# Kernel tuning notes

Hardware: AMD Instinct MI355X
Metric: run time of the kernel (lower is better)

The kernel has to match this reference:

```python
import jax, jax.numpy as jnp
import numpy as np

B, T, C = 8, 1024, 1024   # batch, seq (== block_size), n_embed
H, D = 16, 64             # num_heads, head_size


def setup_inputs() -> dict:
    key = jax.random.key(0)
    kx, kq, kk, kv = jax.random.split(key, 4)
    scale = C ** -0.5  # mimic nn.Linear init scale roughly
    return {
        "x": jax.random.normal(kx, (B, T, C), dtype=jnp.float32),
        "Wq": jax.random.normal(kq, (H, C, D), dtype=jnp.float32) * scale,
        "Wk": jax.random.normal(kk, (H, C, D), dtype=jnp.float32) * scale,
        "Wv": jax.random.normal(kv, (H, C, D), dtype=jnp.float32) * scale,
    }


def reference(x, Wq, Wk, Wv):
    # Per-head Q/K/V projections (batched over heads instead of a Python loop)
    q = jnp.einsum("btc,hcd->bhtd", x, Wq)
    k = jnp.einsum("btc,hcd->bhtd", x, Wk)
    v = jnp.einsum("btc,hcd->bhtd", x, Wv)

    # scaled causal attention scores: [B, H, T, T]
    scores = jnp.einsum("bhtd,bhsd->bhts", q, k) * (D ** -0.5)
    causal = jnp.tril(jnp.ones((T, T), dtype=bool))
    scores = jnp.where(causal, scores, jnp.finfo(scores.dtype).min)
    attn = jax.nn.softmax(scores, axis=-1)

    out = jnp.einsum("bhts,bhsd->bhtd", attn, v)  # [B, H, T, D]
    # concat heads along last dim -> [B, T, H*D]
    return out.transpose(0, 2, 1, 3).reshape(B, T, H * D)
```

## Files before the change

kernel.cpp:

```cpp
#include <hip/hip_runtime.h>
#include <hip/hip_bf16.h>
#include <cstdint>


typedef __attribute__((ext_vector_type(8))) short short8;
typedef __attribute__((ext_vector_type(4))) short bfs4;
typedef __attribute__((ext_vector_type(4))) float f32x4;

typedef const __attribute__((address_space(1))) void* gas1_t;
typedef __attribute__((address_space(3))) void* las3_t;

__device__ __forceinline__ void gl_lds16(const void* g, void* l) {
  __builtin_amdgcn_global_load_lds((gas1_t)g, (las3_t)l, 16, 0, 0);
}

__device__ __forceinline__ unsigned short f2bf(float f) {
  union { float f; unsigned int u; } v; v.f = f;
  unsigned int u = v.u;
  return (unsigned short)((u + 0x7fffu + ((u >> 16) & 1u)) >> 16);
}

__device__ __forceinline__ unsigned int pk_bf16(float a, float b) {
  union { __hip_bfloat162 h; unsigned int u; } cv;
  cv.h = __float22bfloat162_rn(make_float2(a, b));
  return cv.u;
}

__global__ __launch_bounds__(256) void k_convert_x(const float* __restrict__ x,
                                                   unsigned short* __restrict__ xb) {
  int g = blockIdx.x * 256 + threadIdx.x;
  const float4* xp = (const float4*)x + (size_t)g * 2;
  float4 a = xp[0], b = xp[1];
  short8 o;
  o[0] = (short)f2bf(a.x); o[1] = (short)f2bf(a.y);
  o[2] = (short)f2bf(a.z); o[3] = (short)f2bf(a.w);
  o[4] = (short)f2bf(b.x); o[5] = (short)f2bf(b.y);
  o[6] = (short)f2bf(b.z); o[7] = (short)f2bf(b.w);
  *(short8*)(xb + (size_t)g * 8) = o;
}

__global__ __launch_bounds__(256) void k_convert_w(const float* __restrict__ Wq,
                                                   const float* __restrict__ Wk,
                                                   const float* __restrict__ Wv,
                                                   unsigned short* __restrict__ Wt) {
  int g = blockIdx.x * 256 + threadIdx.x;
  int d  = g & 63;
  int cb = (g >> 6) & 127;
  int h  = (g >> 13) & 15;
  int p  = g >> 17;
  const float* W = (p == 0) ? Wq : (p == 1) ? Wk : Wv;
  const float* src = W + ((size_t)h * 1024 + cb * 8) * 64 + d;
  short8 o;
#pragma unroll
  for (int j = 0; j < 8; ++j) o[j] = (short)f2bf(src[(size_t)j * 64]);
  *(short8*)(Wt + (((size_t)p * 16 + h) * 64 + d) * 1024 + cb * 8) = o;
}

__global__ __launch_bounds__(256) void k_proj(const unsigned short* __restrict__ xb,
                                              const unsigned short* __restrict__ Wt,
                                              unsigned short* __restrict__ Qb,
                                              unsigned short* __restrict__ Kb,
                                              unsigned short* __restrict__ Vt) {
  __shared__ alignas(16) unsigned short As[8192];
  __shared__ alignas(16) unsigned short Bs[8192];
  const int p   = blockIdx.y;
  const int bx  = blockIdx.x;
  const int tid = threadIdx.x;
  const int lane = tid & 63, w = tid >> 6;
  const int ln = lane & 15, quad = lane >> 4;
  const int wm = w >> 1, wn = w & 1;

  const unsigned short* Abase;
  const unsigned short* Bbase;
  int m0, n0;
  const int c = bx & 7, j = bx >> 3;
  if (p < 2) {
    Abase = xb; Bbase = Wt + (size_t)p * 1048576;
    m0 = ((j >> 3) * 8 + c) * 128;
    n0 = (j & 7) * 128;
  } else {
    Abase = Wt + (size_t)2 * 1048576; Bbase = xb;
    n0 = ((j >> 3) * 8 + c) * 128;
    m0 = (j & 7) * 128;
  }

  f32x4 acc[4][4];
#pragma unroll
  for (int i = 0; i < 4; ++i)
#pragma unroll
    for (int jj = 0; jj < 4; ++jj) acc[i][jj] = (f32x4){0.f, 0.f, 0.f, 0.f};

  for (int kt = 0; kt < 16; ++kt) {
    const int c0 = kt * 64;
    __syncthreads();
#pragma unroll
    for (int i = 0; i < 4; ++i) {
      int idx = i * 256 + tid;
      int iln = idx & 15, iq = (idx >> 4) & 3, imt = (idx >> 6) & 7, ikk = (idx >> 9) & 1;
      int row = imt * 16 + iln;
      int col = c0 + ikk * 32 + iq * 8;
      char* la = (char*)As + (size_t)(i * 256 + (tid & ~63)) * 16;
      char* lb = (char*)Bs + (size_t)(i * 256 + (tid & ~63)) * 16;
      gl_lds16(Abase + (size_t)(m0 + row) * 1024 + col, la);
      gl_lds16(Bbase + (size_t)(n0 + row) * 1024 + col, lb);
    }
    __builtin_amdgcn_s_waitcnt(0);
    __syncthreads();

    short8 af[2][4], bfr[2][4];
#pragma unroll
    for (int kk = 0; kk < 2; ++kk)
#pragma unroll
      for (int t4 = 0; t4 < 4; ++t4) {
        af[kk][t4]  = *(const short8*)&As[(size_t)((((kk * 8 + wm * 4 + t4) * 4 + quad) * 16 + ln)) * 8];
        bfr[kk][t4] = *(const short8*)&Bs[(size_t)((((kk * 8 + wn * 4 + t4) * 4 + quad) * 16 + ln)) * 8];
      }
#pragma unroll
    for (int kk = 0; kk < 2; ++kk)
#pragma unroll
      for (int mt = 0; mt < 4; ++mt)
#pragma unroll
        for (int nt = 0; nt < 4; ++nt)
          acc[mt][nt] = __builtin_amdgcn_mfma_f32_16x16x32_bf16(
              af[kk][mt], bfr[kk][nt], acc[mt][nt], 0, 0, 0);
  }

  unsigned short* outp = (p == 0) ? Qb : (p == 1) ? Kb : Vt;
#pragma unroll
  for (int mt = 0; mt < 4; ++mt)
#pragma unroll
    for (int nt = 0; nt < 4; ++nt)
#pragma unroll
      for (int r = 0; r < 4; ++r) {
        int m = m0 + (wm * 4 + mt) * 16 + quad * 4 + r;
        int n = n0 + (wn * 4 + nt) * 16 + ln;
        size_t addr;
        if (p < 2) {
          addr = ((size_t)(m >> 10) * 16 + (n >> 6)) * 65536 + (size_t)(m & 1023) * 64 + (n & 63);
        } else {
          addr = ((size_t)(n >> 10) * 1024 + m) * 1024 + (n & 1023);
        }
        outp[addr] = f2bf(acc[mt][nt][r]);
      }
}

__global__ __launch_bounds__(256) void k_attn(const unsigned short* __restrict__ Qb,
                                              const unsigned short* __restrict__ Kb,
                                              const unsigned short* __restrict__ Vt,
                                              float* __restrict__ out) {
  __shared__ alignas(16) unsigned short Ks[4096];
  __shared__ alignas(16) unsigned short Vs[4096];
  __shared__ alignas(16) unsigned short Ps[8192];
  const int bid = blockIdx.x;
  const int qb = 7 - (bid >> 7);
  const int bh = bid & 127;
  const int b = bh >> 4, h = bh & 15;
  const int tid = threadIdx.x, lane = tid & 63, w = tid >> 6;
  const int ln = lane & 15, quad = lane >> 4;

  short8 qf[2][2];
#pragma unroll
  for (int qt = 0; qt < 2; ++qt) {
    const int q = qb * 128 + qt * 64 + w * 16 + ln;
#pragma unroll
    for (int kk = 0; kk < 2; ++kk)
      qf[qt][kk] = *(const short8*)(Qb + ((size_t)bh * 1024 + q) * 64 + kk * 32 + quad * 8);
  }

  f32x4 o[2][4];
#pragma unroll
  for (int qt = 0; qt < 2; ++qt)
#pragma unroll
    for (int dt = 0; dt < 4; ++dt) o[qt][dt] = (f32x4){0.f, 0.f, 0.f, 0.f};
  float l_i[2] = {0.f, 0.f};
  const float sc = 0.18033688011112042f;
  const float FM = 16.0f;

  const int ktmax = 2 * qb + 1;
  for (int kt = 0; kt <= ktmax; ++kt) {
    const int s0 = kt * 64;
    __syncthreads();
#pragma unroll
    for (int i = 0; i < 2; ++i) {
      int idx = i * 256 + tid;
      int iln = idx & 15, iq = (idx >> 4) & 3, ikk = (idx >> 6) & 1, it = (idx >> 7) & 3;
      char* lk = (char*)Ks + (size_t)(i * 256 + (tid & ~63)) * 16;
      char* lv = (char*)Vs + (size_t)(i * 256 + (tid & ~63)) * 16;
      gl_lds16(Kb + ((size_t)bh * 1024 + s0 + it * 16 + iln) * 64 + ikk * 32 + iq * 8, lk);
      gl_lds16(Vt + ((size_t)bh * 64 + it * 16 + iln) * 1024 + s0 + ikk * 32 + iq * 8, lv);
    }
    __builtin_amdgcn_s_waitcnt(0);
    __syncthreads();

    f32x4 st[2][4];
#pragma unroll
    for (int s = 0; s < 4; ++s) {
      st[0][s] = (f32x4){0.f, 0.f, 0.f, 0.f};
      st[1][s] = (f32x4){0.f, 0.f, 0.f, 0.f};
#pragma unroll
      for (int kk = 0; kk < 2; ++kk) {
        short8 kf = *(const short8*)&Ks[(size_t)(((s * 2 + kk) * 4 + quad) * 16 + ln) * 8];
        st[0][s] = __builtin_amdgcn_mfma_f32_16x16x32_bf16(kf, qf[0][kk], st[0][s], 0, 0, 0);
        st[1][s] = __builtin_amdgcn_mfma_f32_16x16x32_bf16(kf, qf[1][kk], st[1][s], 0, 0, 0);
      }
    }

#pragma unroll
    for (int qt = 0; qt < 2; ++qt) {
      const int q = qb * 128 + qt * 64 + w * 16 + ln;
      const bool masked = (kt >= 2 * qb + qt);
      float pv[4][4];
      float rs = 0.f;
#pragma unroll
      for (int s = 0; s < 4; ++s)
#pragma unroll
        for (int r = 0; r < 4; ++r) {
          float v = fmaf(st[qt][s][r], sc, -FM);
          if (masked) {
            int sidx = s0 + s * 16 + quad * 4 + r;
            if (sidx > q) v = -1.0e30f;
          }
          float e = __builtin_amdgcn_exp2f(v);
          pv[s][r] = e;
          rs += e;
        }
      rs += __shfl_xor(rs, 16);
      rs += __shfl_xor(rs, 32);
      l_i[qt] += rs;

      unsigned short* Pq = Ps + (w * 2 + qt) * 1024;
#pragma unroll
      for (int s = 0; s < 4; ++s) {
        union { bfs4 v; unsigned int u[2]; } pk;
        pk.u[0] = pk_bf16(pv[s][0], pv[s][1]);
        pk.u[1] = pk_bf16(pv[s][2], pv[s][3]);
        *(bfs4*)&Pq[(s * 2 + (quad >> 1)) * 128 + ln * 8 + (quad & 1) * 4] = pk.v;
      }
    }

#pragma unroll
    for (int kk = 0; kk < 2; ++kk) {
      short8 pf0 = *(const short8*)&Ps[(size_t)(w * 2 + 0) * 1024 + (size_t)((kk * 4 + quad) * 16 + ln) * 8];
      short8 pf1 = *(const short8*)&Ps[(size_t)(w * 2 + 1) * 1024 + (size_t)((kk * 4 + quad) * 16 + ln) * 8];
#pragma unroll
      for (int dt = 0; dt < 4; ++dt) {
        short8 vf = *(const short8*)&Vs[(size_t)(((dt * 2 + kk) * 4 + quad) * 16 + ln) * 8];
        o[0][dt] = __builtin_amdgcn_mfma_f32_16x16x32_bf16(vf, pf0, o[0][dt], 0, 0, 0);
        o[1][dt] = __builtin_amdgcn_mfma_f32_16x16x32_bf16(vf, pf1, o[1][dt], 0, 0, 0);
      }
    }
  }

#pragma unroll
  for (int qt = 0; qt < 2; ++qt) {
    const int q = qb * 128 + qt * 64 + w * 16 + ln;
    const float rl = 1.0f / l_i[qt];
#pragma unroll
    for (int dt = 0; dt < 4; ++dt) {
      float4 ov;
      ov.x = o[qt][dt][0] * rl; ov.y = o[qt][dt][1] * rl;
      ov.z = o[qt][dt][2] * rl; ov.w = o[qt][dt][3] * rl;
      *(float4*)(out + ((size_t)b * 1024 + q) * 1024 + h * 64 + dt * 16 + quad * 4) = ov;
    }
  }
}

extern "C" void kernel_launch(void* const* d_in, const int* in_sizes, int n_in,
                              void* d_out, int out_size, void* d_ws, size_t ws_size,
                              hipStream_t stream) {
  const float* x  = (const float*)d_in[0];
  const float* Wq = (const float*)d_in[1];
  const float* Wk = (const float*)d_in[2];
  const float* Wv = (const float*)d_in[3];
  float* out = (float*)d_out;

  unsigned short* ws = (unsigned short*)d_ws;
  unsigned short* xb = ws;
  unsigned short* Wt = ws + 8388608;
  unsigned short* Qb = ws + 11534336;
  unsigned short* Kb = ws + 19922944;
  unsigned short* Vt = ws + 28311552;

  hipLaunchKernelGGL(k_convert_x, dim3(4096), dim3(256), 0, stream, x, xb);
  hipLaunchKernelGGL(k_convert_w, dim3(1536), dim3(256), 0, stream, Wq, Wk, Wv, Wt);
  hipLaunchKernelGGL(k_proj, dim3(512, 3), dim3(256), 0, stream, xb, Wt, Qb, Kb, Vt);
  hipLaunchKernelGGL(k_attn, dim3(1024), dim3(256), 0, stream, Qb, Kb, Vt, out);
}
```

Baseline: 236.0 us.

## Double-buffer LDS tiles in projection and attention kernels to prefetch the next tile

Both the projection GEMM and the attention kernel now keep two LDS buffers for their global-to-LDS tiles. Each loop iteration issues the loads for the next K-tile (or K/V tile) before running the MFMA work on the current one, with a single barrier at the end of the iteration. The goal is to hide global load latency behind matrix compute instead of stalling on a full wait every iteration. In exchange, LDS use per block doubles for the staged tiles, which may lower occupancy. The code also relies on the barrier's implicit memory wait, since the explicit waitcnt is gone.

```diff
diff --git a/kernel.cpp b/kernel.cpp
--- a/kernel.cpp
+++ b/kernel.cpp
@@ -61,8 +61,8 @@
                                               unsigned short* __restrict__ Qb,
                                               unsigned short* __restrict__ Kb,
                                               unsigned short* __restrict__ Vt) {
-  __shared__ alignas(16) unsigned short As[8192];
-  __shared__ alignas(16) unsigned short Bs[8192];
+  __shared__ alignas(16) unsigned short As[2][8192];
+  __shared__ alignas(16) unsigned short Bs[2][8192];
   const int p   = blockIdx.y;
   const int bx  = blockIdx.x;
   const int tid = threadIdx.x;
@@ -84,36 +84,41 @@
     m0 = (j & 7) * 128;
   }
 
-  f32x4 acc[4][4];
-#pragma unroll
-  for (int i = 0; i < 4; ++i)
-#pragma unroll
-    for (int jj = 0; jj < 4; ++jj) acc[i][jj] = (f32x4){0.f, 0.f, 0.f, 0.f};
-
-  for (int kt = 0; kt < 16; ++kt) {
+  auto stage = [&](int kt, int buf) {
     const int c0 = kt * 64;
-    __syncthreads();
 #pragma unroll
     for (int i = 0; i < 4; ++i) {
       int idx = i * 256 + tid;
       int iln = idx & 15, iq = (idx >> 4) & 3, imt = (idx >> 6) & 7, ikk = (idx >> 9) & 1;
       int row = imt * 16 + iln;
       int col = c0 + ikk * 32 + iq * 8;
-      char* la = (char*)As + (size_t)(i * 256 + (tid & ~63)) * 16;
-      char* lb = (char*)Bs + (size_t)(i * 256 + (tid & ~63)) * 16;
+      char* la = (char*)&As[buf][0] + (size_t)(i * 256 + (tid & ~63)) * 16;
+      char* lb = (char*)&Bs[buf][0] + (size_t)(i * 256 + (tid & ~63)) * 16;
       gl_lds16(Abase + (size_t)(m0 + row) * 1024 + col, la);
       gl_lds16(Bbase + (size_t)(n0 + row) * 1024 + col, lb);
     }
-    __builtin_amdgcn_s_waitcnt(0);
-    __syncthreads();
+  };
+
+  f32x4 acc[4][4];
+#pragma unroll
+  for (int i = 0; i < 4; ++i)
+#pragma unroll
+    for (int jj = 0; jj < 4; ++jj) acc[i][jj] = (f32x4){0.f, 0.f, 0.f, 0.f};
+
+  stage(0, 0);
+  __syncthreads();
+
+  for (int kt = 0; kt < 16; ++kt) {
+    const int cur = kt & 1;
+    if (kt < 15) stage(kt + 1, cur ^ 1);
 
     short8 af[2][4], bfr[2][4];
 #pragma unroll
     for (int kk = 0; kk < 2; ++kk)
 #pragma unroll
       for (int t4 = 0; t4 < 4; ++t4) {
-        af[kk][t4]  = *(const short8*)&As[(size_t)((((kk * 8 + wm * 4 + t4) * 4 + quad) * 16 + ln)) * 8];
-        bfr[kk][t4] = *(const short8*)&Bs[(size_t)((((kk * 8 + wn * 4 + t4) * 4 + quad) * 16 + ln)) * 8];
+        af[kk][t4]  = *(const short8*)&As[cur][(size_t)((((kk * 8 + wm * 4 + t4) * 4 + quad) * 16 + ln)) * 8];
+        bfr[kk][t4] = *(const short8*)&Bs[cur][(size_t)((((kk * 8 + wn * 4 + t4) * 4 + quad) * 16 + ln)) * 8];
       }
 #pragma unroll
     for (int kk = 0; kk < 2; ++kk)
@@ -123,6 +128,8 @@
         for (int nt = 0; nt < 4; ++nt)
           acc[mt][nt] = __builtin_amdgcn_mfma_f32_16x16x32_bf16(
               af[kk][mt], bfr[kk][nt], acc[mt][nt], 0, 0, 0);
+
+    __syncthreads();
   }
 
   unsigned short* outp = (p == 0) ? Qb : (p == 1) ? Kb : Vt;
@@ -148,8 +155,8 @@
                                               const unsigned short* __restrict__ Kb,
                                               const unsigned short* __restrict__ Vt,
                                               float* __restrict__ out) {
-  __shared__ alignas(16) unsigned short Ks[4096];
-  __shared__ alignas(16) unsigned short Vs[4096];
+  __shared__ alignas(16) unsigned short Ks[2][4096];
+  __shared__ alignas(16) unsigned short Vs[2][4096];
   __shared__ alignas(16) unsigned short Ps[8192];
   const int bid = blockIdx.x;
   const int qb = 7 - (bid >> 7);
@@ -158,6 +165,19 @@
   const int tid = threadIdx.x, lane = tid & 63, w = tid >> 6;
   const int ln = lane & 15, quad = lane >> 4;
 
+  auto stage = [&](int kt, int buf) {
+    const int s0 = kt * 64;
+#pragma unroll
+    for (int i = 0; i < 2; ++i) {
+      int idx = i * 256 + tid;
+      int iln = idx & 15, iq = (idx >> 4) & 3, ikk = (idx >> 6) & 1, it = (idx >> 7) & 3;
+      char* lk = (char*)&Ks[buf][0] + (size_t)(i * 256 + (tid & ~63)) * 16;
+      char* lv = (char*)&Vs[buf][0] + (size_t)(i * 256 + (tid & ~63)) * 16;
+      gl_lds16(Kb + ((size_t)bh * 1024 + s0 + it * 16 + iln) * 64 + ikk * 32 + iq * 8, lk);
+      gl_lds16(Vt + ((size_t)bh * 64 + it * 16 + iln) * 1024 + s0 + ikk * 32 + iq * 8, lv);
+    }
+  };
+
   short8 qf[2][2];
 #pragma unroll
   for (int qt = 0; qt < 2; ++qt) {
@@ -177,20 +197,13 @@
   const float FM = 16.0f;
 
   const int ktmax = 2 * qb + 1;
+  stage(0, 0);
+  __syncthreads();
+
   for (int kt = 0; kt <= ktmax; ++kt) {
+    const int cur = kt & 1;
     const int s0 = kt * 64;
-    __syncthreads();
-#pragma unroll
-    for (int i = 0; i < 2; ++i) {
-      int idx = i * 256 + tid;
-      int iln = idx & 15, iq = (idx >> 4) & 3, ikk = (idx >> 6) & 1, it = (idx >> 7) & 3;
-      char* lk = (char*)Ks + (size_t)(i * 256 + (tid & ~63)) * 16;
-      char* lv = (char*)Vs + (size_t)(i * 256 + (tid & ~63)) * 16;
-      gl_lds16(Kb + ((size_t)bh * 1024 + s0 + it * 16 + iln) * 64 + ikk * 32 + iq * 8, lk);
-      gl_lds16(Vt + ((size_t)bh * 64 + it * 16 + iln) * 1024 + s0 + ikk * 32 + iq * 8, lv);
-    }
-    __builtin_amdgcn_s_waitcnt(0);
-    __syncthreads();
+    if (kt < ktmax) stage(kt + 1, cur ^ 1);
 
     f32x4 st[2][4];
 #pragma unroll
@@ -199,7 +212,7 @@
       st[1][s] = (f32x4){0.f, 0.f, 0.f, 0.f};
 #pragma unroll
       for (int kk = 0; kk < 2; ++kk) {
-        short8 kf = *(const short8*)&Ks[(size_t)(((s * 2 + kk) * 4 + quad) * 16 + ln) * 8];
+        short8 kf = *(const short8*)&Ks[cur][(size_t)(((s * 2 + kk) * 4 + quad) * 16 + ln) * 8];
         st[0][s] = __builtin_amdgcn_mfma_f32_16x16x32_bf16(kf, qf[0][kk], st[0][s], 0, 0, 0);
         st[1][s] = __builtin_amdgcn_mfma_f32_16x16x32_bf16(kf, qf[1][kk], st[1][s], 0, 0, 0);
       }
@@ -244,11 +257,13 @@
       short8 pf1 = *(const short8*)&Ps[(size_t)(w * 2 + 1) * 1024 + (size_t)((kk * 4 + quad) * 16 + ln) * 8];
 #pragma unroll
       for (int dt = 0; dt < 4; ++dt) {
-        short8 vf = *(const short8*)&Vs[(size_t)(((dt * 2 + kk) * 4 + quad) * 16 + ln) * 8];
+        short8 vf = *(const short8*)&Vs[cur][(size_t)(((dt * 2 + kk) * 4 + quad) * 16 + ln) * 8];
         o[0][dt] = __builtin_amdgcn_mfma_f32_16x16x32_bf16(vf, pf0, o[0][dt], 0, 0, 0);
         o[1][dt] = __builtin_amdgcn_mfma_f32_16x16x32_bf16(vf, pf1, o[1][dt], 0, 0, 0);
       }
     }
+
+    __syncthreads();
   }
 
 #pragma unroll
```

Result: slower. 262.2 us (+11.1%).

## Prefetch next K-tile into registers to overlap global loads with MFMA

Applied to the files above, without the earlier changes.

Replaces the direct global-to-LDS loads in both the projection GEMM and the attention kernel with register-staged loads. The next tile is fetched into registers while the current tile is computed from LDS, then written to LDS at the top of the next iteration. This hides global load latency behind compute instead of stalling on waitcnt(0) each iteration. In exchange it uses more VGPRs, which may lower occupancy, and adds an extra barrier per iteration.

```diff
diff --git a/kernel.cpp b/kernel.cpp
--- a/kernel.cpp
+++ b/kernel.cpp
@@ -6,13 +6,7 @@
 typedef __attribute__((ext_vector_type(8))) short short8;
 typedef __attribute__((ext_vector_type(4))) short bfs4;
 typedef __attribute__((ext_vector_type(4))) float f32x4;
-
-typedef const __attribute__((address_space(1))) void* gas1_t;
-typedef __attribute__((address_space(3))) void* las3_t;
-
-__device__ __forceinline__ void gl_lds16(const void* g, void* l) {
-  __builtin_amdgcn_global_load_lds((gas1_t)g, (las3_t)l, 16, 0, 0);
-}
+typedef __attribute__((ext_vector_type(4))) int   i32x4;
 
 __device__ __forceinline__ unsigned short f2bf(float f) {
   union { float f; unsigned int u; } v; v.f = f;
@@ -84,45 +78,52 @@
     m0 = (j & 7) * 128;
   }
 
-  f32x4 acc[4][4];
-#pragma unroll
-  for (int i = 0; i < 4; ++i)
-#pragma unroll
-    for (int jj = 0; jj < 4; ++jj) acc[i][jj] = (f32x4){0.f, 0.f, 0.f, 0.f};
-
-  for (int kt = 0; kt < 16; ++kt) {
+  i32x4 ra[4], rb[4];
+  auto ld = [&](int kt) {
     const int c0 = kt * 64;
-    __syncthreads();
 #pragma unroll
     for (int i = 0; i < 4; ++i) {
       int idx = i * 256 + tid;
       int iln = idx & 15, iq = (idx >> 4) & 3, imt = (idx >> 6) & 7, ikk = (idx >> 9) & 1;
       int row = imt * 16 + iln;
       int col = c0 + ikk * 32 + iq * 8;
-      char* la = (char*)As + (size_t)(i * 256 + (tid & ~63)) * 16;
-      char* lb = (char*)Bs + (size_t)(i * 256 + (tid & ~63)) * 16;
-      gl_lds16(Abase + (size_t)(m0 + row) * 1024 + col, la);
-      gl_lds16(Bbase + (size_t)(n0 + row) * 1024 + col, lb);
-    }
-    __builtin_amdgcn_s_waitcnt(0);
+      ra[i] = *(const i32x4*)(Abase + (size_t)(m0 + row) * 1024 + col);
+      rb[i] = *(const i32x4*)(Bbase + (size_t)(n0 + row) * 1024 + col);
+    }
+  };
+
+  f32x4 acc[4][4];
+#pragma unroll
+  for (int i = 0; i < 4; ++i)
+#pragma unroll
+    for (int jj = 0; jj < 4; ++jj) acc[i][jj] = (f32x4){0.f, 0.f, 0.f, 0.f};
+
+  ld(0);
+  for (int kt = 0; kt < 16; ++kt) {
+#pragma unroll
+    for (int i = 0; i < 4; ++i) {
+      *(i32x4*)((char*)As + (size_t)(i * 256 + tid) * 16) = ra[i];
+      *(i32x4*)((char*)Bs + (size_t)(i * 256 + tid) * 16) = rb[i];
+    }
     __syncthreads();
-
-    short8 af[2][4], bfr[2][4];
-#pragma unroll
-    for (int kk = 0; kk < 2; ++kk)
+    if (kt < 15) ld(kt + 1);
+
+#pragma unroll
+    for (int kk = 0; kk < 2; ++kk) {
+      short8 af[4], bfr[4];
 #pragma unroll
       for (int t4 = 0; t4 < 4; ++t4) {
-        af[kk][t4]  = *(const short8*)&As[(size_t)((((kk * 8 + wm * 4 + t4) * 4 + quad) * 16 + ln)) * 8];
-        bfr[kk][t4] = *(const short8*)&Bs[(size_t)((((kk * 8 + wn * 4 + t4) * 4 + quad) * 16 + ln)) * 8];
-      }
-#pragma unroll
-    for (int kk = 0; kk < 2; ++kk)
+        af[t4]  = *(const short8*)&As[(size_t)((((kk * 8 + wm * 4 + t4) * 4 + quad) * 16 + ln)) * 8];
+        bfr[t4] = *(const short8*)&Bs[(size_t)((((kk * 8 + wn * 4 + t4) * 4 + quad) * 16 + ln)) * 8];
+      }
 #pragma unroll
       for (int mt = 0; mt < 4; ++mt)
 #pragma unroll
         for (int nt = 0; nt < 4; ++nt)
           acc[mt][nt] = __builtin_amdgcn_mfma_f32_16x16x32_bf16(
-              af[kk][mt], bfr[kk][nt], acc[mt][nt], 0, 0, 0);
+              af[mt], bfr[nt], acc[mt][nt], 0, 0, 0);
+    }
+    __syncthreads();
   }
 
   unsigned short* outp = (p == 0) ? Qb : (p == 1) ? Kb : Vt;
@@ -158,6 +159,18 @@
   const int tid = threadIdx.x, lane = tid & 63, w = tid >> 6;
   const int ln = lane & 15, quad = lane >> 4;
 
+  i32x4 rk[2], rv[2];
+  auto ldkv = [&](int kt) {
+    const int s0 = kt * 64;
+#pragma unroll
+    for (int i = 0; i < 2; ++i) {
+      int idx = i * 256 + tid;
+      int iln = idx & 15, iq = (idx >> 4) & 3, ikk = (idx >> 6) & 1, it = (idx >> 7) & 3;
+      rk[i] = *(const i32x4*)(Kb + ((size_t)bh * 1024 + s0 + it * 16 + iln) * 64 + ikk * 32 + iq * 8);
+      rv[i] = *(const i32x4*)(Vt + ((size_t)bh * 64 + it * 16 + iln) * 1024 + s0 + ikk * 32 + iq * 8);
+    }
+  };
+
   short8 qf[2][2];
 #pragma unroll
   for (int qt = 0; qt < 2; ++qt) {
@@ -177,20 +190,17 @@
   const float FM = 16.0f;
 
   const int ktmax = 2 * qb + 1;
+  ldkv(0);
+
   for (int kt = 0; kt <= ktmax; ++kt) {
     const int s0 = kt * 64;
+#pragma unroll
+    for (int i = 0; i < 2; ++i) {
+      *(i32x4*)((char*)Ks + (size_t)(i * 256 + tid) * 16) = rk[i];
+      *(i32x4*)((char*)Vs + (size_t)(i * 256 + tid) * 16) = rv[i];
+    }
     __syncthreads();
-#pragma unroll
-    for (int i = 0; i < 2; ++i) {
-      int idx = i * 256 + tid;
-      int iln = idx & 15, iq = (idx >> 4) & 3, ikk = (idx >> 6) & 1, it = (idx >> 7) & 3;
-      char* lk = (char*)Ks + (size_t)(i * 256 + (tid & ~63)) * 16;
-      char* lv = (char*)Vs + (size_t)(i * 256 + (tid & ~63)) * 16;
-      gl_lds16(Kb + ((size_t)bh * 1024 + s0 + it * 16 + iln) * 64 + ikk * 32 + iq * 8, lk);
-      gl_lds16(Vt + ((size_t)bh * 64 + it * 16 + iln) * 1024 + s0 + ikk * 32 + iq * 8, lv);
-    }
-    __builtin_amdgcn_s_waitcnt(0);
-    __syncthreads();
+    if (kt < ktmax) ldkv(kt + 1);
 
     f32x4 st[2][4];
 #pragma unroll
@@ -249,6 +259,8 @@
         o[1][dt] = __builtin_amdgcn_mfma_f32_16x16x32_bf16(vf, pf1, o[1][dt], 0, 0, 0);
       }
     }
+
+    __syncthreads();
   }
 
 #pragma unroll
```

Result: no change. 232.1 us (-1.6%).
